# Performance work log

Hardware: AMD Instinct MI355X
Metric: run time of the kernel (lower is better)

The kernel has to match this reference:

```python
import jax, jax.numpy as jnp
import numpy as np
from jax import lax

RGB_H, RGB_W = 288, 256
FOV = 64.0
CAMERA_YAWS = (-60.0, 0.0, 60.0)
CAMERA_X, CAMERA_Z = 1.4, 2.5
MAX_POOL_KS = 7
MAX_DET = 15
NEG_BIG = 100000.0


def _cam_matrices():
    # Intrinsics (same formula as CoordConverter)
    focal = RGB_W / (2.0 * np.tan(FOV * np.pi / 360.0))
    K = np.eye(3, dtype=np.float32)
    K[0, 0] = K[1, 1] = focal
    K[0, 2] = RGB_W / 2.0
    K[1, 2] = RGB_H / 2.0
    # lidar -> world: pure translation by lidar_xyz = [0, 0, camera_z]
    L2W = np.eye(4, dtype=np.float32)
    L2W[2, 3] = CAMERA_Z
    # world -> cam: inverse of (translation cam_xyz, yaw rotation about z)
    W2Cs = []
    for yaw in CAMERA_YAWS:
        r = np.deg2rad(yaw)
        c, s = np.cos(r), np.sin(r)
        M = np.eye(4, dtype=np.float32)
        M[:3, :3] = np.array([[c, -s, 0.0], [s, c, 0.0], [0.0, 0.0, 1.0]], dtype=np.float32)
        M[:3, 3] = np.array([CAMERA_X, 0.0, CAMERA_Z], dtype=np.float32)
        inv = np.eye(4, dtype=np.float32)
        inv[:3, :3] = M[:3, :3].T
        inv[:3, 3] = -M[:3, :3].T @ M[:3, 3]
        W2Cs.append(inv)
    return K, L2W, np.stack(W2Cs)


def setup_inputs() -> dict:
    key = jax.random.key(0)
    k1, k2, k3 = jax.random.split(key, 3)
    N = 2_000_000
    lidar = jax.random.normal(k1, (N, 4), dtype=jnp.float32) * 15.0  # xyz spread ~ tens of meters
    sems = jax.random.uniform(k2, (3, 10, RGB_H, RGB_W), dtype=jnp.float32)
    heatmaps = jax.random.uniform(k3, (2, 640, 640), dtype=jnp.float32)
    K, L2W, W2C = _cam_matrices()
    return {
        "lidar": lidar,
        "sems": sems,
        "heatmaps": heatmaps,
        "K": jnp.asarray(K),
        "lidar_to_world": jnp.asarray(L2W),
        "world_to_cam": jnp.asarray(W2C),
    }


def _project(lidar, K, L2W, W2C):
    # lidar: [N,4] -> integer (u, v, z) camera coords, truncation like torch .long()
    xyz1 = jnp.concatenate([lidar[:, :3], jnp.ones_like(lidar[:, :1])], axis=-1).T  # [4,N]
    world = L2W @ xyz1                                   # [4,N]
    cam = W2C @ world                                    # [4,N]
    cam3 = jnp.stack([cam[1], -cam[2], cam[0]], axis=0)  # [3,N]
    c2 = K @ cam3                                        # [3,N]
    z = 1e-5 + c2[2]
    uvz = jnp.stack([c2[0] / z, c2[1] / z, c2[2]], axis=0).T  # [N,3]
    return uvz.astype(jnp.int32)


def _point_painting(lidar, sems, K, L2W, W2Cs):
    n_cam, sem_c, sem_h, sem_w = sems.shape
    N = lidar.shape[0]
    painted = jnp.zeros((N, sem_c), dtype=lidar.dtype)
    # sequential per-camera overwrite, matching the torch loop semantics
    for i in range(n_cam):
        uvz = _project(lidar, K, L2W, W2Cs[i])
        u, v, z = uvz[:, 0], uvz[:, 1], uvz[:, 2]
        valid = (z >= 0) & (u >= 0) & (u < sem_w) & (v >= 0) & (v < sem_h)
        uc = jnp.clip(u, 0, sem_w - 1)
        vc = jnp.clip(v, 0, sem_h - 1)
        gathered = sems[i][:, vc, uc].T  # [N, sem_c]
        painted = jnp.where(valid[:, None], gathered, painted)
    return painted


def _extract_peak(hm):
    # 7x7 stride-1 max pool with SAME padding, suppress non-peaks, top-k
    mx = lax.reduce_window(hm, -jnp.inf, lax.max,
                           (MAX_POOL_KS, MAX_POOL_KS), (1, 1), "SAME")
    possible = hm - (mx > hm).astype(hm.dtype) * NEG_BIG
    score, loc = lax.top_k(possible.reshape(-1), MAX_DET)
    return score, loc


def reference(lidar, sems, heatmaps, K, lidar_to_world, world_to_cam):
    painted = _point_painting(lidar, sems, K, lidar_to_world, world_to_cam)
    scores, locs = jax.vmap(_extract_peak)(heatmaps)  # [n_cls, 15] each
    return painted, scores, locs
```

## Files before the change

kernel.cpp:

```cpp
#include <hip/hip_runtime.h>
#include <hip/hip_bf16.h>
#include <float.h>
#include <math.h>

#define RGB_H 288
#define RGB_W 256
#define NCH 10
#define NCH_PAD 12
#define HM_N 2
#define HM_S 640
#define MAX_DET_K 15
#define IPT 4
#define PBLK (256 * IPT)

typedef float f4 __attribute__((ext_vector_type(4)));
typedef float f2 __attribute__((ext_vector_type(2)));

#define TW 64
#define TH 16
#define SW (TW + 6)
#define SP 72
#define SH (TH + 6)
#define NTILE_X (HM_S / TW)
#define NTILE_Y (HM_S / TH)
#define TILES_PER_MAP (NTILE_X * NTILE_Y)
#define S1N (TILES_PER_MAP * MAX_DET_K)
#define RPT 24

#define TP_TOTAL (3 * RGB_H * RGB_W)
#define TP_BLOCKS ((TP_TOTAL + 255) / 256)
#define PEAK_BLOCKS (TILES_PER_MAP * HM_N)

#define WS_S1SCORE  0
#define WS_S1IDX    (WS_S1SCORE + HM_N * S1N * 4)
#define WS_PSEMS    ((WS_S1IDX + HM_N * S1N * 4 + 15) & ~15)
#define PSEMS_BYTES ((size_t)TP_TOTAL * NCH_PAD * 4)

__global__ __launch_bounds__(256) void prep_kernel(
    const float* __restrict__ sems,
    const float* __restrict__ hm,
    float* __restrict__ ps,
    float* __restrict__ s1score,
    int* __restrict__ s1idx,
    int use_ps)
{
    const int bid = blockIdx.x;
    const int tid = threadIdx.x;

    __shared__ float sA[SH * SP];
    __shared__ float hx[SH * TW];
    __shared__ float lsc[TW * TH];
    __shared__ int   lix[TW * TH];
    __shared__ int   lcnt;

    if (bid >= PEAK_BLOCKS) {
        const int t = (bid - PEAK_BLOCKS) * 256 + tid;
        if (t >= TP_TOTAL) return;
        const int u = t & (RGB_W - 1);
        const int v = (t >> 8) % RGB_H;
        const int cam = t / (RGB_H * RGB_W);
        float vals[NCH_PAD];
#pragma unroll
        for (int c = 0; c < NCH; ++c)
            vals[c] = sems[(((long long)cam * NCH + c) * RGB_H + v) * RGB_W + u];
        vals[10] = 0.0f; vals[11] = 0.0f;
        f4* dst = (f4*)(ps + (size_t)t * NCH_PAD);
        dst[0] = (f4){vals[0], vals[1], vals[2],  vals[3]};
        dst[1] = (f4){vals[4], vals[5], vals[6],  vals[7]};
        dst[2] = (f4){vals[8], vals[9], vals[10], vals[11]};
        return;
    }

    const int m  = bid / TILES_PER_MAP;
    const int tt = bid % TILES_PER_MAP;
    const int gx0 = (tt % NTILE_X) * TW;
    const int gy0 = (tt / NTILE_X) * TH;
    const int tx = tid & 63;
    const int ty = tid >> 6;
    const float* h = hm + (long long)m * HM_S * HM_S;

    if (tid == 0) lcnt = 0;
    __syncthreads();

    for (int yy = ty; yy < SH; yy += 4) {
        const int gv = gy0 + yy - 3;
        const bool vok = (gv >= 0) & (gv < HM_S);
        for (int xx = tx; xx < SW; xx += 64) {
            const int gu = gx0 + xx - 3;
            float val = -INFINITY;
            if (vok & (gu >= 0) & (gu < HM_S)) val = h[gv * HM_S + gu];
            sA[yy * SP + xx] = val;
        }
    }
    __syncthreads();

    for (int yy = ty; yy < SH; yy += 4) {
        const float* r = sA + yy * SP + tx;
        float mx = r[0];
#pragma unroll
        for (int k = 1; k < 7; ++k) mx = fmaxf(mx, r[k]);
        hx[yy * TW + tx] = mx;
    }
    __syncthreads();

    for (int ry = ty; ry < TH; ry += 4) {
        const float val = sA[(ry + 3) * SP + tx + 3];
        float mx = hx[ry * TW + tx];
#pragma unroll
        for (int k = 1; k < 7; ++k) mx = fmaxf(mx, hx[(ry + k) * TW + tx]);
        if (!(mx > val)) {
            int pos = atomicAdd(&lcnt, 1);
            lsc[pos] = val;
            lix[pos] = (gy0 + ry) * HM_S + (gx0 + tx);
        }
    }
    __syncthreads();

    if (tid < 64) {
        const int n = lcnt;
        const int slot0 = (m * TILES_PER_MAP + tt) * MAX_DET_K;
        for (int t = 0; t < MAX_DET_K; ++t) {
            float bs = -INFINITY; int bi = 0x7fffffff; int bp = -1;
            for (int j = tid; j < n; j += 64) {
                const float s = lsc[j]; const int id = lix[j];
                if (s > bs || (s == bs && id < bi)) { bs = s; bi = id; bp = j; }
            }
#pragma unroll
            for (int off = 32; off > 0; off >>= 1) {
                const float os = __shfl_down(bs, off);
                const int   oi = __shfl_down(bi, off);
                const int   op = __shfl_down(bp, off);
                if (os > bs || (os == bs && oi < bi)) { bs = os; bi = oi; bp = op; }
            }
            bs = __shfl(bs, 0); bi = __shfl(bi, 0); bp = __shfl(bp, 0);
            if (tid == 0) {
                s1score[slot0 + t] = bs;
                s1idx[slot0 + t]   = bi;
                if (bp >= 0) lsc[bp] = -INFINITY;
            }
        }
    }
}

__global__ __launch_bounds__(256) void main_kernel(
    const float* __restrict__ lidar,
    const float* __restrict__ sems,
    const float* __restrict__ psems,
    int use_ps,
    const float* __restrict__ Km,
    const float* __restrict__ L2W,
    const float* __restrict__ W2C,
    float* __restrict__ out,
    int N,
    const float* __restrict__ s1score,
    const int* __restrict__ s1idx,
    float* __restrict__ out_scores,
    float* __restrict__ out_locs)
{
    const int tid = threadIdx.x;

    if (blockIdx.x < HM_N) {
        const int m = blockIdx.x;
        const int lane = tid & 63;
        const int wv = tid >> 6;

        float es[RPT]; int ei[RPT];
#pragma unroll
        for (int e = 0; e < RPT; ++e) {
            const int j = e * 256 + tid;
            if (j < S1N) { es[e] = s1score[m * S1N + j]; ei[e] = s1idx[m * S1N + j]; }
            else         { es[e] = -INFINITY;            ei[e] = 0x7fffffff; }
        }

        __shared__ float bss[4];
        __shared__ int   bis[4];
        __shared__ int   bps[4];
        __shared__ int   fbp;

        for (int t = 0; t < MAX_DET_K; ++t) {
            float bs = -INFINITY; int bi = 0x7fffffff; int bp = -1;
#pragma unroll
            for (int e = 0; e < RPT; ++e) {
                if (es[e] > bs || (es[e] == bs && ei[e] < bi)) {
                    bs = es[e]; bi = ei[e]; bp = e * 256 + tid;
                }
            }
#pragma unroll
            for (int off = 32; off > 0; off >>= 1) {
                const float os = __shfl_down(bs, off);
                const int   oi = __shfl_down(bi, off);
                const int   op = __shfl_down(bp, off);
                if (os > bs || (os == bs && oi < bi)) { bs = os; bi = oi; bp = op; }
            }
            if (lane == 0) { bss[wv] = bs; bis[wv] = bi; bps[wv] = bp; }
            __syncthreads();
            if (tid == 0) {
                float s = bss[0]; int i0 = bis[0]; int p = bps[0];
#pragma unroll
                for (int w = 1; w < 4; ++w) {
                    if (bss[w] > s || (bss[w] == s && bis[w] < i0)) {
                        s = bss[w]; i0 = bis[w]; p = bps[w];
                    }
                }
                out_scores[m * MAX_DET_K + t] = s;
                out_locs[m * MAX_DET_K + t]   = (float)i0;
                fbp = p;
            }
            __syncthreads();
            const int wbp = fbp;
            if (wbp >= 0 && (wbp & 255) == tid) es[wbp >> 8] = -INFINITY;
            __syncthreads();
        }
        return;
    }

    const long long base = (long long)(blockIdx.x - HM_N) * PBLK;

    long long gofs[IPT];
#pragma unroll
    for (int k = 0; k < IPT; ++k) {
        const long long p = base + k * 256 + tid;
        f4 pt = (f4){0.f, 0.f, 0.f, 0.f};
        if (p < N) pt = __builtin_nontemporal_load(((const f4*)lidar) + p);
        const float x = pt.x, y = pt.y, z = pt.z;

        float w[3];
#pragma unroll
        for (int i = 0; i < 3; ++i) {
            float acc = L2W[4*i+0] * x;
            acc = fmaf(L2W[4*i+1], y, acc);
            acc = fmaf(L2W[4*i+2], z, acc);
            acc = fmaf(L2W[4*i+3], 1.0f, acc);
            w[i] = acc;
        }

        int sel = -1, su = 0, sv = 0;
#pragma unroll
        for (int i = 0; i < 3; ++i) {
            const float* W = W2C + 16 * i;
            float cam[3];
#pragma unroll
            for (int r = 0; r < 3; ++r) {
                float acc = W[4*r+0] * w[0];
                acc = fmaf(W[4*r+1], w[1], acc);
                acc = fmaf(W[4*r+2], w[2], acc);
                acc = fmaf(W[4*r+3], 1.0f, acc);
                cam[r] = acc;
            }
            const float c30 = cam[1], c31 = -cam[2], c32 = cam[0];
            float pr[3];
#pragma unroll
            for (int r = 0; r < 3; ++r) {
                float acc = Km[3*r+0] * c30;
                acc = fmaf(Km[3*r+1], c31, acc);
                acc = fmaf(Km[3*r+2], c32, acc);
                pr[r] = acc;
            }
            const float zz = 1e-5f + pr[2];
            const int u  = __float2int_rz(pr[0] / zz);
            const int v  = __float2int_rz(pr[1] / zz);
            const int zi = __float2int_rz(pr[2]);
            const bool valid = (zi >= 0) & (u >= 0) & (u < RGB_W)
                             & (v >= 0) & (v < RGB_H);
            if (valid) { sel = i; su = u; sv = v; }
        }
        gofs[k] = (sel >= 0)
                ? ((long long)sel * RGB_H + sv) * RGB_W + su
                : -1;
        if (p >= N) gofs[k] = -2;
    }

    f4 ga[IPT], gb[IPT]; f2 gc[IPT];
    if (use_ps) {
#pragma unroll
        for (int k = 0; k < IPT; ++k) {
            ga[k] = (f4){0,0,0,0}; gb[k] = (f4){0,0,0,0}; gc[k] = (f2){0,0};
            if (gofs[k] >= 0) {
                const f4* g = (const f4*)(psems + gofs[k] * NCH_PAD);
                ga[k] = g[0]; gb[k] = g[1];
                const f2* g2 = (const f2*)(g + 2);
                gc[k] = g2[0];
            }
        }
    } else {
#pragma unroll
        for (int k = 0; k < IPT; ++k) {
            ga[k] = (f4){0,0,0,0}; gb[k] = (f4){0,0,0,0}; gc[k] = (f2){0,0};
            if (gofs[k] >= 0) {
                const int sel = (int)(gofs[k] / (RGB_H * RGB_W));
                const int pix = (int)(gofs[k] % (RGB_H * RGB_W));
                const float* s = sems + ((long long)sel * NCH) * RGB_H * RGB_W + pix;
                const long long pl = (long long)RGB_H * RGB_W;
                ga[k] = (f4){s[0], s[pl], s[2*pl], s[3*pl]};
                gb[k] = (f4){s[4*pl], s[5*pl], s[6*pl], s[7*pl]};
                gc[k] = (f2){s[8*pl], s[9*pl]};
            }
        }
    }

#pragma unroll
    for (int k = 0; k < IPT; ++k) {
        const long long p = base + k * 256 + tid;
        if (gofs[k] == -2) continue;
        f2* o = (f2*)(out + p * NCH);
        o[0] = (f2){ga[k].x, ga[k].y};
        o[1] = (f2){ga[k].z, ga[k].w};
        o[2] = (f2){gb[k].x, gb[k].y};
        o[3] = (f2){gb[k].z, gb[k].w};
        o[4] = gc[k];
    }
}

extern "C" void kernel_launch(void* const* d_in, const int* in_sizes, int n_in,
                              void* d_out, int out_size, void* d_ws, size_t ws_size,
                              hipStream_t stream)
{
    const float* lidar = (const float*)d_in[0];
    const float* sems  = (const float*)d_in[1];
    const float* hm    = (const float*)d_in[2];
    const float* Km    = (const float*)d_in[3];
    const float* L2W   = (const float*)d_in[4];
    const float* W2C   = (const float*)d_in[5];
    float* out = (float*)d_out;
    const int N = in_sizes[0] / 4;

    char* ws = (char*)d_ws;
    float* s1score = (float*)(ws + WS_S1SCORE);
    int*   s1idx   = (int*)(ws + WS_S1IDX);
    float* psems   = (float*)(ws + WS_PSEMS);
    const int use_ps = (ws_size >= (size_t)WS_PSEMS + PSEMS_BYTES) ? 1 : 0;

    const int k1_blocks = PEAK_BLOCKS + (use_ps ? TP_BLOCKS : 0);
    prep_kernel<<<k1_blocks, 256, 0, stream>>>(sems, hm, psems, s1score, s1idx, use_ps);

    float* out_scores = out + (long long)N * NCH;
    float* out_locs   = out_scores + HM_N * MAX_DET_K;
    const int paint_blocks = (int)((N + PBLK - 1) / PBLK);
    main_kernel<<<HM_N + paint_blocks, 256, 0, stream>>>(
        lidar, sems, psems, use_ps, Km, L2W, W2C, out, N,
        s1score, s1idx, out_scores, out_locs);
}
```

Measured before the change: 156.4 us.

## Move peak-tile stage into main kernel with last-block merge via atomic counter

Moves the heatmap max-pool and per-tile top-k work out of the prep kernel into the main kernel, where it runs alongside the painting blocks. The final merge is done by whichever tile block finishes last for each map, detected through a global atomic done-counter with thread fences. The prep kernel now only builds the transposed semantics table and resets the counters. This shortens the prep kernel and drops the separate merge blocks that had to wait on prior results. The cost is extra shared memory in main_kernel, which can lower occupancy for the painting blocks, and reliance on fence and atomic ordering for correctness.

```diff
diff --git a/kernel.cpp b/kernel.cpp
--- a/kernel.cpp
+++ b/kernel.cpp
@@ -33,113 +33,32 @@
 
 #define WS_S1SCORE  0
 #define WS_S1IDX    (WS_S1SCORE + HM_N * S1N * 4)
-#define WS_PSEMS    ((WS_S1IDX + HM_N * S1N * 4 + 15) & ~15)
+#define WS_DONE     (WS_S1IDX + HM_N * S1N * 4)
+#define WS_PSEMS    ((WS_DONE + 16 + 63) & ~63)
 #define PSEMS_BYTES ((size_t)TP_TOTAL * NCH_PAD * 4)
 
 __global__ __launch_bounds__(256) void prep_kernel(
     const float* __restrict__ sems,
-    const float* __restrict__ hm,
     float* __restrict__ ps,
-    float* __restrict__ s1score,
-    int* __restrict__ s1idx,
+    int* __restrict__ done,
     int use_ps)
 {
-    const int bid = blockIdx.x;
-    const int tid = threadIdx.x;
-
-    __shared__ float sA[SH * SP];
-    __shared__ float hx[SH * TW];
-    __shared__ float lsc[TW * TH];
-    __shared__ int   lix[TW * TH];
-    __shared__ int   lcnt;
-
-    if (bid >= PEAK_BLOCKS) {
-        const int t = (bid - PEAK_BLOCKS) * 256 + tid;
-        if (t >= TP_TOTAL) return;
-        const int u = t & (RGB_W - 1);
-        const int v = (t >> 8) % RGB_H;
-        const int cam = t / (RGB_H * RGB_W);
-        float vals[NCH_PAD];
-#pragma unroll
-        for (int c = 0; c < NCH; ++c)
-            vals[c] = sems[(((long long)cam * NCH + c) * RGB_H + v) * RGB_W + u];
-        vals[10] = 0.0f; vals[11] = 0.0f;
-        f4* dst = (f4*)(ps + (size_t)t * NCH_PAD);
-        dst[0] = (f4){vals[0], vals[1], vals[2],  vals[3]};
-        dst[1] = (f4){vals[4], vals[5], vals[6],  vals[7]};
-        dst[2] = (f4){vals[8], vals[9], vals[10], vals[11]};
-        return;
-    }
-
-    const int m  = bid / TILES_PER_MAP;
-    const int tt = bid % TILES_PER_MAP;
-    const int gx0 = (tt % NTILE_X) * TW;
-    const int gy0 = (tt / NTILE_X) * TH;
-    const int tx = tid & 63;
-    const int ty = tid >> 6;
-    const float* h = hm + (long long)m * HM_S * HM_S;
-
-    if (tid == 0) lcnt = 0;
-    __syncthreads();
-
-    for (int yy = ty; yy < SH; yy += 4) {
-        const int gv = gy0 + yy - 3;
-        const bool vok = (gv >= 0) & (gv < HM_S);
-        for (int xx = tx; xx < SW; xx += 64) {
-            const int gu = gx0 + xx - 3;
-            float val = -INFINITY;
-            if (vok & (gu >= 0) & (gu < HM_S)) val = h[gv * HM_S + gu];
-            sA[yy * SP + xx] = val;
-        }
-    }
-    __syncthreads();
-
-    for (int yy = ty; yy < SH; yy += 4) {
-        const float* r = sA + yy * SP + tx;
-        float mx = r[0];
-#pragma unroll
-        for (int k = 1; k < 7; ++k) mx = fmaxf(mx, r[k]);
-        hx[yy * TW + tx] = mx;
-    }
-    __syncthreads();
-
-    for (int ry = ty; ry < TH; ry += 4) {
-        const float val = sA[(ry + 3) * SP + tx + 3];
-        float mx = hx[ry * TW + tx];
-#pragma unroll
-        for (int k = 1; k < 7; ++k) mx = fmaxf(mx, hx[(ry + k) * TW + tx]);
-        if (!(mx > val)) {
-            int pos = atomicAdd(&lcnt, 1);
-            lsc[pos] = val;
-            lix[pos] = (gy0 + ry) * HM_S + (gx0 + tx);
-        }
-    }
-    __syncthreads();
-
-    if (tid < 64) {
-        const int n = lcnt;
-        const int slot0 = (m * TILES_PER_MAP + tt) * MAX_DET_K;
-        for (int t = 0; t < MAX_DET_K; ++t) {
-            float bs = -INFINITY; int bi = 0x7fffffff; int bp = -1;
-            for (int j = tid; j < n; j += 64) {
-                const float s = lsc[j]; const int id = lix[j];
-                if (s > bs || (s == bs && id < bi)) { bs = s; bi = id; bp = j; }
-            }
-#pragma unroll
-            for (int off = 32; off > 0; off >>= 1) {
-                const float os = __shfl_down(bs, off);
-                const int   oi = __shfl_down(bi, off);
-                const int   op = __shfl_down(bp, off);
-                if (os > bs || (os == bs && oi < bi)) { bs = os; bi = oi; bp = op; }
-            }
-            bs = __shfl(bs, 0); bi = __shfl(bi, 0); bp = __shfl(bp, 0);
-            if (tid == 0) {
-                s1score[slot0 + t] = bs;
-                s1idx[slot0 + t]   = bi;
-                if (bp >= 0) lsc[bp] = -INFINITY;
-            }
-        }
-    }
+    if (blockIdx.x == 0 && threadIdx.x < HM_N) done[threadIdx.x] = 0;
+    if (!use_ps) return;
+    const int t = blockIdx.x * 256 + threadIdx.x;
+    if (t >= TP_TOTAL) return;
+    const int u = t & (RGB_W - 1);
+    const int v = (t >> 8) % RGB_H;
+    const int cam = t / (RGB_H * RGB_W);
+    float vals[NCH_PAD];
+#pragma unroll
+    for (int c = 0; c < NCH; ++c)
+        vals[c] = sems[(((long long)cam * NCH + c) * RGB_H + v) * RGB_W + u];
+    vals[10] = 0.0f; vals[11] = 0.0f;
+    f4* dst = (f4*)(ps + (size_t)t * NCH_PAD);
+    dst[0] = (f4){vals[0], vals[1], vals[2],  vals[3]};
+    dst[1] = (f4){vals[4], vals[5], vals[6],  vals[7]};
+    dst[2] = (f4){vals[8], vals[9], vals[10], vals[11]};
 }
 
 __global__ __launch_bounds__(256) void main_kernel(
@@ -150,71 +69,161 @@
     const float* __restrict__ Km,
     const float* __restrict__ L2W,
     const float* __restrict__ W2C,
+    const float* __restrict__ hm,
     float* __restrict__ out,
     int N,
-    const float* __restrict__ s1score,
-    const int* __restrict__ s1idx,
+    float* s1score,
+    int* s1idx,
+    int* done,
     float* __restrict__ out_scores,
     float* __restrict__ out_locs)
 {
     const int tid = threadIdx.x;
 
-    if (blockIdx.x < HM_N) {
-        const int m = blockIdx.x;
-        const int lane = tid & 63;
-        const int wv = tid >> 6;
-
-        float es[RPT]; int ei[RPT];
-#pragma unroll
-        for (int e = 0; e < RPT; ++e) {
-            const int j = e * 256 + tid;
-            if (j < S1N) { es[e] = s1score[m * S1N + j]; ei[e] = s1idx[m * S1N + j]; }
-            else         { es[e] = -INFINITY;            ei[e] = 0x7fffffff; }
-        }
-
-        __shared__ float bss[4];
-        __shared__ int   bis[4];
-        __shared__ int   bps[4];
-        __shared__ int   fbp;
-
-        for (int t = 0; t < MAX_DET_K; ++t) {
-            float bs = -INFINITY; int bi = 0x7fffffff; int bp = -1;
+    if (blockIdx.x < PEAK_BLOCKS) {
+        __shared__ float sA[SH * SP];
+        __shared__ float hx[SH * TW];
+        __shared__ float lsc[TW * TH];
+        __shared__ int   lix[TW * TH];
+        __shared__ int   lcnt;
+        __shared__ int   do_merge;
+
+        const int bid = blockIdx.x;
+        const int m  = bid / TILES_PER_MAP;
+        const int tt = bid % TILES_PER_MAP;
+        const int gx0 = (tt % NTILE_X) * TW;
+        const int gy0 = (tt / NTILE_X) * TH;
+        const int tx = tid & 63;
+        const int ty = tid >> 6;
+        const float* h = hm + (long long)m * HM_S * HM_S;
+
+        if (tid == 0) lcnt = 0;
+        __syncthreads();
+
+        for (int yy = ty; yy < SH; yy += 4) {
+            const int gv = gy0 + yy - 3;
+            const bool vok = (gv >= 0) & (gv < HM_S);
+            for (int xx = tx; xx < SW; xx += 64) {
+                const int gu = gx0 + xx - 3;
+                float val = -INFINITY;
+                if (vok & (gu >= 0) & (gu < HM_S)) val = h[gv * HM_S + gu];
+                sA[yy * SP + xx] = val;
+            }
+        }
+        __syncthreads();
+
+        for (int yy = ty; yy < SH; yy += 4) {
+            const float* r = sA + yy * SP + tx;
+            float mx = r[0];
+#pragma unroll
+            for (int k = 1; k < 7; ++k) mx = fmaxf(mx, r[k]);
+            hx[yy * TW + tx] = mx;
+        }
+        __syncthreads();
+
+        for (int ry = ty; ry < TH; ry += 4) {
+            const float val = sA[(ry + 3) * SP + tx + 3];
+            float mx = hx[ry * TW + tx];
+#pragma unroll
+            for (int k = 1; k < 7; ++k) mx = fmaxf(mx, hx[(ry + k) * TW + tx]);
+            if (!(mx > val)) {
+                int pos = atomicAdd(&lcnt, 1);
+                lsc[pos] = val;
+                lix[pos] = (gy0 + ry) * HM_S + (gx0 + tx);
+            }
+        }
+        __syncthreads();
+
+        if (tid < 64) {
+            const int n = lcnt;
+            const int slot0 = (m * TILES_PER_MAP + tt) * MAX_DET_K;
+            for (int t = 0; t < MAX_DET_K; ++t) {
+                float bs = -INFINITY; int bi = 0x7fffffff; int bp = -1;
+                for (int j = tid; j < n; j += 64) {
+                    const float s = lsc[j]; const int id = lix[j];
+                    if (s > bs || (s == bs && id < bi)) { bs = s; bi = id; bp = j; }
+                }
+#pragma unroll
+                for (int off = 32; off > 0; off >>= 1) {
+                    const float os = __shfl_down(bs, off);
+                    const int   oi = __shfl_down(bi, off);
+                    const int   op = __shfl_down(bp, off);
+                    if (os > bs || (os == bs && oi < bi)) { bs = os; bi = oi; bp = op; }
+                }
+                bs = __shfl(bs, 0); bi = __shfl(bi, 0); bp = __shfl(bp, 0);
+                if (tid == 0) {
+                    s1score[slot0 + t] = bs;
+                    s1idx[slot0 + t]   = bi;
+                    if (bp >= 0) lsc[bp] = -INFINITY;
+                }
+            }
+        }
+        __syncthreads();
+
+        if (tid == 0) {
+            __threadfence();
+            const int d = atomicAdd(&done[m], 1);
+            do_merge = (d == TILES_PER_MAP - 1);
+        }
+        __syncthreads();
+        if (!do_merge) return;
+        __threadfence();
+
+        {
+            const int lane = tid & 63;
+            const int wv = tid >> 6;
+            float es[RPT]; int ei[RPT];
 #pragma unroll
             for (int e = 0; e < RPT; ++e) {
-                if (es[e] > bs || (es[e] == bs && ei[e] < bi)) {
-                    bs = es[e]; bi = ei[e]; bp = e * 256 + tid;
-                }
-            }
-#pragma unroll
-            for (int off = 32; off > 0; off >>= 1) {
-                const float os = __shfl_down(bs, off);
-                const int   oi = __shfl_down(bi, off);
-                const int   op = __shfl_down(bp, off);
-                if (os > bs || (os == bs && oi < bi)) { bs = os; bi = oi; bp = op; }
-            }
-            if (lane == 0) { bss[wv] = bs; bis[wv] = bi; bps[wv] = bp; }
-            __syncthreads();
-            if (tid == 0) {
-                float s = bss[0]; int i0 = bis[0]; int p = bps[0];
-#pragma unroll
-                for (int w = 1; w < 4; ++w) {
-                    if (bss[w] > s || (bss[w] == s && bis[w] < i0)) {
-                        s = bss[w]; i0 = bis[w]; p = bps[w];
+                const int j = e * 256 + tid;
+                if (j < S1N) { es[e] = s1score[m * S1N + j]; ei[e] = s1idx[m * S1N + j]; }
+                else         { es[e] = -INFINITY;            ei[e] = 0x7fffffff; }
+            }
+
+            __shared__ float bss[4];
+            __shared__ int   bis[4];
+            __shared__ int   bps[4];
+            __shared__ int   fbp;
+
+            for (int t = 0; t < MAX_DET_K; ++t) {
+                float bs = -INFINITY; int bi = 0x7fffffff; int bp = -1;
+#pragma unroll
+                for (int e = 0; e < RPT; ++e) {
+                    if (es[e] > bs || (es[e] == bs && ei[e] < bi)) {
+                        bs = es[e]; bi = ei[e]; bp = e * 256 + tid;
                     }
                 }
-                out_scores[m * MAX_DET_K + t] = s;
-                out_locs[m * MAX_DET_K + t]   = (float)i0;
-                fbp = p;
-            }
-            __syncthreads();
-            const int wbp = fbp;
-            if (wbp >= 0 && (wbp & 255) == tid) es[wbp >> 8] = -INFINITY;
-            __syncthreads();
+#pragma unroll
+                for (int off = 32; off > 0; off >>= 1) {
+                    const float os = __shfl_down(bs, off);
+                    const int   oi = __shfl_down(bi, off);
+                    const int   op = __shfl_down(bp, off);
+                    if (os > bs || (os == bs && oi < bi)) { bs = os; bi = oi; bp = op; }
+                }
+                if (lane == 0) { bss[wv] = bs; bis[wv] = bi; bps[wv] = bp; }
+                __syncthreads();
+                if (tid == 0) {
+                    float s = bss[0]; int i0 = bis[0]; int p = bps[0];
+#pragma unroll
+                    for (int w = 1; w < 4; ++w) {
+                        if (bss[w] > s || (bss[w] == s && bis[w] < i0)) {
+                            s = bss[w]; i0 = bis[w]; p = bps[w];
+                        }
+                    }
+                    out_scores[m * MAX_DET_K + t] = s;
+                    out_locs[m * MAX_DET_K + t]   = (float)i0;
+                    fbp = p;
+                }
+                __syncthreads();
+                const int wbp = fbp;
+                if (wbp >= 0 && (wbp & 255) == tid) es[wbp >> 8] = -INFINITY;
+                __syncthreads();
+            }
         }
         return;
     }
 
-    const long long base = (long long)(blockIdx.x - HM_N) * PBLK;
+    const long long base = (long long)(blockIdx.x - PEAK_BLOCKS) * PBLK;
 
     long long gofs[IPT];
 #pragma unroll
@@ -327,16 +336,16 @@
     char* ws = (char*)d_ws;
     float* s1score = (float*)(ws + WS_S1SCORE);
     int*   s1idx   = (int*)(ws + WS_S1IDX);
+    int*   done    = (int*)(ws + WS_DONE);
     float* psems   = (float*)(ws + WS_PSEMS);
     const int use_ps = (ws_size >= (size_t)WS_PSEMS + PSEMS_BYTES) ? 1 : 0;
 
-    const int k1_blocks = PEAK_BLOCKS + (use_ps ? TP_BLOCKS : 0);
-    prep_kernel<<<k1_blocks, 256, 0, stream>>>(sems, hm, psems, s1score, s1idx, use_ps);
+    prep_kernel<<<TP_BLOCKS, 256, 0, stream>>>(sems, psems, done, use_ps);
 
     float* out_scores = out + (long long)N * NCH;
     float* out_locs   = out_scores + HM_N * MAX_DET_K;
     const int paint_blocks = (int)((N + PBLK - 1) / PBLK);
-    main_kernel<<<HM_N + paint_blocks, 256, 0, stream>>>(
-        lidar, sems, psems, use_ps, Km, L2W, W2C, out, N,
-        s1score, s1idx, out_scores, out_locs);
+    main_kernel<<<PEAK_BLOCKS + paint_blocks, 256, 0, stream>>>(
+        lidar, sems, psems, use_ps, Km, L2W, W2C, hm, out, N,
+        s1score, s1idx, done, out_scores, out_locs);
 }
```

New measurement: 196.2 us. +25.5%, slower.
